# Performance work log

Hardware: AMD Instinct MI355X
Metric: run time of the kernel (lower is better)

The kernel has to match this reference:

```python
import jax, jax.numpy as jnp
import numpy as np

LN_EPS = 1e-5

def setup_inputs() -> dict:
    key = jax.random.key(0)
    k1, k2, k3, k4 = jax.random.split(key, 4)
    B, C_ct, C_b, N = 2, 128, 32, 180
    D = H = W = 24
    ct_feat = jax.random.normal(k1, (B, C_ct, D, H, W), dtype=jnp.float32)
    beam_stack = jax.random.normal(k2, (B, N, C_b, D, H, W), dtype=jnp.float32)
    # 1x1x1 Conv3d query projection == per-voxel linear map C_ct -> C_b
    q_w = jax.random.normal(k3, (C_b, C_ct), dtype=jnp.float32) * (1.0 / np.sqrt(C_ct))
    q_b = jnp.zeros((C_b,), dtype=jnp.float32)
    ln_gamma = jnp.ones((C_b,), dtype=jnp.float32)
    ln_beta = jnp.zeros((C_b,), dtype=jnp.float32)
    return {"ct_feat": ct_feat, "beam_stack": beam_stack, "q_w": q_w,
            "q_b": q_b, "ln_gamma": ln_gamma, "ln_beta": ln_beta}

def reference(ct_feat, beam_stack, q_w, q_b, ln_gamma, ln_beta):
    B, C_ct, D, H, W = ct_feat.shape
    _, N, C_b = beam_stack.shape[:3]
    V = D * H * W
    scale = C_b ** -0.5
    # query: 1x1x1 conv -> [B, V, C_b]
    q = jnp.einsum('oc,bcv->bvo', q_w, ct_feat.reshape(B, C_ct, V)) + q_b
    kv = beam_stack.reshape(B, N, C_b, V)  # [B, N, C_b, V]
    # per-voxel logits over N control points
    logits = jnp.einsum('bvc,bncv->bvn', q, kv) * scale  # [B, V, N]
    attn_w = jax.nn.softmax(logits, axis=-1)
    fused = jnp.einsum('bvn,bncv->bvc', attn_w, kv)  # [B, V, C_b]
    # LayerNorm over channel dim (eps matches torch default)
    mu = jnp.mean(fused, axis=-1, keepdims=True)
    var = jnp.mean(jnp.square(fused - mu), axis=-1, keepdims=True)
    fused = (fused - mu) * jax.lax.rsqrt(var + LN_EPS) * ln_gamma + ln_beta
    fused = fused.transpose(0, 2, 1).reshape(B, C_b, D, H, W)
    return fused, attn_w
```

## Files before the change

kernel.cpp:

```cpp
#include <hip/hip_runtime.h>
#include <math.h>

#define BB      2
#define C_CT    128
#define CB      32
#define NN      180
#define VV      13824
#define VOXB    64
#define GR      4
#define NPG     45
#define THREADS 256

typedef float vfloat4 __attribute__((ext_vector_type(4)));

__global__ __launch_bounds__(THREADS, 2)
void vmat_attn_kernel(const float* __restrict__ ct, const float* __restrict__ beam,
                      const float* __restrict__ qw, const float* __restrict__ qb,
                      const float* __restrict__ gam, const float* __restrict__ bet,
                      float* __restrict__ out)
{
    __shared__ __align__(16) float Wbuf[NN * VOXB];
    __shared__ __align__(16) float Pbuf[GR][CB][VOXB];
    __shared__ __align__(16) float l_part[GR][VOXB];
    __shared__ float l_final[VOXB];
    __shared__ float qb_s[CB], gam_s[CB], bet_s[CB];

    const int t    = threadIdx.x;
    const int lane = t & 63;
    const int g    = t >> 6;
    const int vq   = lane & 15;
    const int cg   = lane >> 4;
    const int bid  = blockIdx.x;
    const int b    = bid / (VV / VOXB);
    const int v0   = (bid % (VV / VOXB)) * VOXB;

    for (int i = t; i < CB * C_CT; i += THREADS) Wbuf[i] = qw[i];
    if (t < CB) { qb_s[t] = qb[t]; gam_s[t] = gam[t]; bet_s[t] = bet[t]; }
    __syncthreads();

    {
        const int v = v0 + lane;
        const float* ctp = ct + ((size_t)b * C_CT + g * 32) * VV + v;
        float ctv[32];
        #pragma unroll
        for (int j = 0; j < 32; ++j) ctv[j] = ctp[(size_t)j * VV];
        float qp[CB];
        #pragma unroll
        for (int o = 0; o < CB; ++o) qp[o] = 0.f;
        for (int j = 0; j < 32; ++j) {
            #pragma unroll
            for (int o = 0; o < CB; ++o)
                qp[o] = fmaf(Wbuf[o * C_CT + g * 32 + j], ctv[j], qp[o]);
        }
        #pragma unroll
        for (int o = 0; o < CB; ++o) Pbuf[g][o][lane] = qp[o];
    }
    __syncthreads();

    float q[8][4];
    #pragma unroll
    for (int ci = 0; ci < 8; ++ci) {
        const int o = cg * 8 + ci;
        float4 a0 = *reinterpret_cast<const float4*>(&Pbuf[0][o][vq * 4]);
        float4 a1 = *reinterpret_cast<const float4*>(&Pbuf[1][o][vq * 4]);
        float4 a2 = *reinterpret_cast<const float4*>(&Pbuf[2][o][vq * 4]);
        float4 a3 = *reinterpret_cast<const float4*>(&Pbuf[3][o][vq * 4]);
        q[ci][0] = a0.x + a1.x + a2.x + a3.x + qb_s[o];
        q[ci][1] = a0.y + a1.y + a2.y + a3.y + qb_s[o];
        q[ci][2] = a0.z + a1.z + a2.z + a3.z + qb_s[o];
        q[ci][3] = a0.w + a1.w + a2.w + a3.w + qb_s[o];
    }
    __syncthreads();

    const float scale = 0.17677669529663687f;
    float acc[8][4];
    #pragma unroll
    for (int ci = 0; ci < 8; ++ci)
        acc[ci][0] = acc[ci][1] = acc[ci][2] = acc[ci][3] = 0.f;
    float l0 = 0.f, l1 = 0.f, l2 = 0.f, l3 = 0.f;
    const float* bp0 = beam + (((size_t)b * NN + g * NPG) * CB + cg * 8) * VV + v0 + vq * 4;

    vfloat4 kvA[8], kvB[8];
    auto loadK = [&](vfloat4* kv, int i) {
        const float* bp = bp0 + (size_t)i * CB * VV;
        #pragma unroll
        for (int ci = 0; ci < 8; ++ci)
            kv[ci] = __builtin_nontemporal_load(
                reinterpret_cast<const vfloat4*>(bp + (size_t)ci * VV));
    };
    auto computeK = [&](const vfloat4* kv, int i) {
        float p0 = 0.f, p1 = 0.f, p2 = 0.f, p3 = 0.f;
        #pragma unroll
        for (int ci = 0; ci < 8; ++ci) {
            p0 = fmaf(q[ci][0], kv[ci].x, p0);
            p1 = fmaf(q[ci][1], kv[ci].y, p1);
            p2 = fmaf(q[ci][2], kv[ci].z, p2);
            p3 = fmaf(q[ci][3], kv[ci].w, p3);
        }
        p0 += __shfl_xor(p0, 16); p1 += __shfl_xor(p1, 16);
        p2 += __shfl_xor(p2, 16); p3 += __shfl_xor(p3, 16);
        p0 += __shfl_xor(p0, 32); p1 += __shfl_xor(p1, 32);
        p2 += __shfl_xor(p2, 32); p3 += __shfl_xor(p3, 32);
        float w0 = __expf(fminf(p0 * scale, 60.f));
        float w1 = __expf(fminf(p1 * scale, 60.f));
        float w2 = __expf(fminf(p2 * scale, 60.f));
        float w3 = __expf(fminf(p3 * scale, 60.f));
        if (cg == 0) {
            float4 wv; wv.x = w0; wv.y = w1; wv.z = w2; wv.w = w3;
            *reinterpret_cast<float4*>(&Wbuf[(g * NPG + i) * VOXB + vq * 4]) = wv;
        }
        l0 += w0; l1 += w1; l2 += w2; l3 += w3;
        #pragma unroll
        for (int ci = 0; ci < 8; ++ci) {
            acc[ci][0] = fmaf(w0, kv[ci].x, acc[ci][0]);
            acc[ci][1] = fmaf(w1, kv[ci].y, acc[ci][1]);
            acc[ci][2] = fmaf(w2, kv[ci].z, acc[ci][2]);
            acc[ci][3] = fmaf(w3, kv[ci].w, acc[ci][3]);
        }
    };

    loadK(kvA, 0);
    #pragma unroll 1
    for (int i = 0; i < NPG - 1; i += 2) {
        loadK(kvB, i + 1);
        computeK(kvA, i);
        if (i + 2 < NPG) loadK(kvA, i + 2);
        computeK(kvB, i + 1);
    }
    computeK(kvA, NPG - 1);

    #pragma unroll
    for (int ci = 0; ci < 8; ++ci) {
        float4 av; av.x = acc[ci][0]; av.y = acc[ci][1]; av.z = acc[ci][2]; av.w = acc[ci][3];
        *reinterpret_cast<float4*>(&Pbuf[g][cg * 8 + ci][vq * 4]) = av;
    }
    if (cg == 0) {
        float4 lv; lv.x = l0; lv.y = l1; lv.z = l2; lv.w = l3;
        *reinterpret_cast<float4*>(&l_part[g][vq * 4]) = lv;
    }
    __syncthreads();

    if (t < VOXB) {
        float lt = l_part[0][t] + l_part[1][t] + l_part[2][t] + l_part[3][t];
        l_final[t] = lt;
        float inv_l = 1.f / lt;
        float f[CB], mu = 0.f;
        #pragma unroll
        for (int c = 0; c < CB; ++c) {
            f[c] = (Pbuf[0][c][t] + Pbuf[1][c][t] + Pbuf[2][c][t] + Pbuf[3][c][t]) * inv_l;
            mu += f[c];
        }
        mu *= (1.f / CB);
        float var = 0.f;
        #pragma unroll
        for (int c = 0; c < CB; ++c) { float d = f[c] - mu; var = fmaf(d, d, var); }
        float rs = rsqrtf(var * (1.f / CB) + 1e-5f);
        float* op = out + (size_t)b * CB * VV + v0 + t;
        #pragma unroll
        for (int c = 0; c < CB; ++c)
            op[(size_t)c * VV] = (f[c] - mu) * rs * gam_s[c] + bet_s[c];
    }
    __syncthreads();

    {
        const int vv = t & 63;
        const int j  = t >> 6;
        const float inv_l = 1.f / l_final[vv];
        float* arow = out + (size_t)BB * CB * VV + ((size_t)b * VV + v0 + vv) * NN;
        const int q4_begin = j * 12;
        const int q4_end   = (j == 3) ? 45 : (j * 12 + 12);
        for (int q4 = q4_begin; q4 < q4_end; ++q4) {
            const int n0 = q4 * 4;
            float4 val;
            val.x = Wbuf[(n0 + 0) * VOXB + vv] * inv_l;
            val.y = Wbuf[(n0 + 1) * VOXB + vv] * inv_l;
            val.z = Wbuf[(n0 + 2) * VOXB + vv] * inv_l;
            val.w = Wbuf[(n0 + 3) * VOXB + vv] * inv_l;
            *reinterpret_cast<float4*>(arow + n0) = val;
        }
    }
}

extern "C" void kernel_launch(void* const* d_in, const int* in_sizes, int n_in,
                              void* d_out, int out_size, void* d_ws, size_t ws_size,
                              hipStream_t stream) {
    (void)in_sizes; (void)n_in; (void)out_size; (void)d_ws; (void)ws_size;
    const float* ct   = (const float*)d_in[0];
    const float* beam = (const float*)d_in[1];
    const float* qw   = (const float*)d_in[2];
    const float* qb   = (const float*)d_in[3];
    const float* gam  = (const float*)d_in[4];
    const float* bet  = (const float*)d_in[5];
    float* out = (float*)d_out;
    dim3 grid(BB * (VV / VOXB));
    vmat_attn_kernel<<<grid, THREADS, 0, stream>>>(ct, beam, qw, qb, gam, bet, out);
}
```

Measured before the change: 142.6 us.

## Split fused attention into projection, streaming, and combine kernels via workspace

Splits the single fused kernel into three: a query-projection kernel, a 64-thread streaming kernel that handles one quarter of the control points per block, and a combine kernel that merges partial accumulators, applies LayerNorm and normalizes attention weights in place. The goal is to raise the number of blocks and wavefronts in flight so more beam-stack loads are outstanding, and the streaming loop moves to triple buffering. The cost is extra global traffic: queries are staged in the output buffer, and partials plus unnormalized weights take an extra round trip through memory. If the workspace is too small, the original fused kernel runs as a fallback.

After: 191.4 us. 34.3% more time.

```diff
diff --git a/kernel.cpp b/kernel.cpp
--- a/kernel.cpp
+++ b/kernel.cpp
@@ -6,38 +6,229 @@
 #define CB      32
 #define NN      180
 #define VV      13824
-#define VOXB    64
-#define GR      4
 #define NPG     45
-#define THREADS 256
+#define SCALE   0.17677669529663687f
 
 typedef float vfloat4 __attribute__((ext_vector_type(4)));
 
-__global__ __launch_bounds__(THREADS, 2)
-void vmat_attn_kernel(const float* __restrict__ ct, const float* __restrict__ beam,
-                      const float* __restrict__ qw, const float* __restrict__ qb,
-                      const float* __restrict__ gam, const float* __restrict__ bet,
-                      float* __restrict__ out)
+__global__ __launch_bounds__(256, 2)
+void qproj_kernel(const float* __restrict__ ct, const float* __restrict__ qw,
+                  const float* __restrict__ qb, float* __restrict__ qout)
 {
-    __shared__ __align__(16) float Wbuf[NN * VOXB];
-    __shared__ __align__(16) float Pbuf[GR][CB][VOXB];
-    __shared__ __align__(16) float l_part[GR][VOXB];
-    __shared__ float l_final[VOXB];
+    __shared__ float qw_t[C_CT * 33];
+    __shared__ __align__(16) float ct_s[C_CT * 64];
+    __shared__ float q_s[64 * 33];
+    __shared__ float qb_s[CB];
+    const int t  = threadIdx.x;
+    const int b  = blockIdx.x / 216;
+    const int v0 = (blockIdx.x % 216) * 64;
+
+    for (int i = t; i < CB * C_CT; i += 256) {
+        const int o = i >> 7, c = i & 127;
+        qw_t[c * 33 + o] = qw[i];
+    }
+    {
+        const float* ctbase = ct + (size_t)b * C_CT * VV + v0;
+        for (int i = t; i < C_CT * 16; i += 256) {
+            const int c = i >> 4, k = i & 15;
+            *reinterpret_cast<vfloat4*>(&ct_s[c * 64 + k * 4]) =
+                *reinterpret_cast<const vfloat4*>(ctbase + (size_t)c * VV + k * 4);
+        }
+    }
+    if (t < CB) qb_s[t] = qb[t];
+    __syncthreads();
+
+    const int o = t & 31, va = t >> 5;
+    float a[8];
+    #pragma unroll
+    for (int k = 0; k < 8; ++k) a[k] = qb_s[o];
+    for (int kc = 0; kc < C_CT; ++kc) {
+        const float wk = qw_t[kc * 33 + o];
+        const float* cr = &ct_s[kc * 64];
+        #pragma unroll
+        for (int k = 0; k < 8; ++k) a[k] = fmaf(wk, cr[va + 8 * k], a[k]);
+    }
+    #pragma unroll
+    for (int k = 0; k < 8; ++k) q_s[(va + 8 * k) * 33 + o] = a[k];
+    __syncthreads();
+
+    for (int i = t; i < CB * 64; i += 256) {
+        const int c = i >> 6, v = i & 63;
+        qout[((size_t)b * CB + c) * VV + v0 + v] = q_s[v * 33 + c];
+    }
+}
+
+__global__ __launch_bounds__(64, 2)
+void stream_kernel(const float* __restrict__ beam, const float* __restrict__ qarr,
+                   float* __restrict__ wout, float* __restrict__ ws_acc,
+                   float* __restrict__ ws_l)
+{
+    const int u  = blockIdx.x;
+    const int b  = u / 864;
+    const int r  = u % 864;
+    const int g  = r & 3;
+    const int v0 = (r >> 2) * 64;
+    const int lane = threadIdx.x;
+    const int vq = lane & 15;
+    const int cg = lane >> 4;
+
+    float q[8][4];
+    #pragma unroll
+    for (int ci = 0; ci < 8; ++ci) {
+        vfloat4 qv = *reinterpret_cast<const vfloat4*>(
+            qarr + ((size_t)b * CB + cg * 8 + ci) * VV + v0 + vq * 4);
+        q[ci][0] = qv.x; q[ci][1] = qv.y; q[ci][2] = qv.z; q[ci][3] = qv.w;
+    }
+
+    float acc[8][4];
+    #pragma unroll
+    for (int ci = 0; ci < 8; ++ci)
+        acc[ci][0] = acc[ci][1] = acc[ci][2] = acc[ci][3] = 0.f;
+    float l0 = 0.f, l1 = 0.f, l2 = 0.f, l3 = 0.f;
+
+    const float* bpc  = beam + (((size_t)b * NN + g * NPG) * CB + cg * 8) * VV + v0 + vq * 4;
+    float*       wrow = wout + ((size_t)b * VV + v0 + vq * 4) * NN + g * NPG;
+
+    vfloat4 kvA[8], kvB[8], kvC[8];
+    auto loadK = [&](vfloat4* kv, int i) {
+        const float* p = bpc + (size_t)i * (CB * VV);
+        #pragma unroll
+        for (int ci = 0; ci < 8; ++ci)
+            kv[ci] = __builtin_nontemporal_load(
+                reinterpret_cast<const vfloat4*>(p + (size_t)ci * VV));
+    };
+    auto computeK = [&](const vfloat4* kv, int i) {
+        float p0 = 0.f, p1 = 0.f, p2 = 0.f, p3 = 0.f;
+        #pragma unroll
+        for (int ci = 0; ci < 8; ++ci) {
+            p0 = fmaf(q[ci][0], kv[ci].x, p0);
+            p1 = fmaf(q[ci][1], kv[ci].y, p1);
+            p2 = fmaf(q[ci][2], kv[ci].z, p2);
+            p3 = fmaf(q[ci][3], kv[ci].w, p3);
+        }
+        p0 += __shfl_xor(p0, 16); p1 += __shfl_xor(p1, 16);
+        p2 += __shfl_xor(p2, 16); p3 += __shfl_xor(p3, 16);
+        p0 += __shfl_xor(p0, 32); p1 += __shfl_xor(p1, 32);
+        p2 += __shfl_xor(p2, 32); p3 += __shfl_xor(p3, 32);
+        const float w0 = __expf(fminf(p0 * SCALE, 60.f));
+        const float w1 = __expf(fminf(p1 * SCALE, 60.f));
+        const float w2 = __expf(fminf(p2 * SCALE, 60.f));
+        const float w3 = __expf(fminf(p3 * SCALE, 60.f));
+        if (cg == 0) {
+            wrow[0 * NN + i] = w0;
+            wrow[1 * NN + i] = w1;
+            wrow[2 * NN + i] = w2;
+            wrow[3 * NN + i] = w3;
+        }
+        l0 += w0; l1 += w1; l2 += w2; l3 += w3;
+        #pragma unroll
+        for (int ci = 0; ci < 8; ++ci) {
+            acc[ci][0] = fmaf(w0, kv[ci].x, acc[ci][0]);
+            acc[ci][1] = fmaf(w1, kv[ci].y, acc[ci][1]);
+            acc[ci][2] = fmaf(w2, kv[ci].z, acc[ci][2]);
+            acc[ci][3] = fmaf(w3, kv[ci].w, acc[ci][3]);
+        }
+    };
+
+    loadK(kvA, 0);
+    loadK(kvB, 1);
+    #pragma unroll 1
+    for (int i = 0; i < NPG; i += 3) {
+        loadK(kvC, i + 2);
+        computeK(kvA, i);
+        if (i + 3 < NPG) loadK(kvA, i + 3);
+        computeK(kvB, i + 1);
+        if (i + 4 < NPG) loadK(kvB, i + 4);
+        computeK(kvC, i + 2);
+    }
+
+    #pragma unroll
+    for (int ci = 0; ci < 8; ++ci) {
+        vfloat4 a; a.x = acc[ci][0]; a.y = acc[ci][1]; a.z = acc[ci][2]; a.w = acc[ci][3];
+        *reinterpret_cast<vfloat4*>(
+            ws_acc + (((size_t)b * 4 + g) * CB + cg * 8 + ci) * VV + v0 + vq * 4) = a;
+    }
+    if (cg == 0) {
+        vfloat4 lv; lv.x = l0; lv.y = l1; lv.z = l2; lv.w = l3;
+        *reinterpret_cast<vfloat4*>(ws_l + ((size_t)b * 4 + g) * VV + v0 + vq * 4) = lv;
+    }
+}
+
+__global__ __launch_bounds__(256, 4)
+void combine_kernel(const float* __restrict__ ws_acc, const float* __restrict__ ws_l,
+                    const float* __restrict__ gam, const float* __restrict__ bet,
+                    float* __restrict__ out)
+{
+    __shared__ float il_s[32];
+    const int t  = threadIdx.x;
+    const int b  = blockIdx.x / 432;
+    const int v0 = (blockIdx.x % 432) * 32;
+
+    if (t < 32) {
+        const int v = v0 + t;
+        float lt = 0.f;
+        #pragma unroll
+        for (int g = 0; g < 4; ++g) lt += ws_l[((size_t)b * 4 + g) * VV + v];
+        const float il = 1.f / lt;
+        il_s[t] = il;
+        float f[CB], mu = 0.f;
+        #pragma unroll
+        for (int c = 0; c < CB; ++c) {
+            float s = 0.f;
+            #pragma unroll
+            for (int g = 0; g < 4; ++g)
+                s += ws_acc[(((size_t)b * 4 + g) * CB + c) * VV + v];
+            f[c] = s * il;
+            mu += f[c];
+        }
+        mu *= (1.f / CB);
+        float var = 0.f;
+        #pragma unroll
+        for (int c = 0; c < CB; ++c) { const float d = f[c] - mu; var = fmaf(d, d, var); }
+        const float rs = rsqrtf(var * (1.f / CB) + 1e-5f);
+        float* op = out + (size_t)b * CB * VV + v;
+        #pragma unroll
+        for (int c = 0; c < CB; ++c)
+            op[(size_t)c * VV] = (f[c] - mu) * rs * gam[c] + bet[c];
+    }
+    __syncthreads();
+
+    {
+        const int v  = t >> 3;
+        const int kk = t & 7;
+        const float il = il_s[v];
+        float* arow = out + (size_t)BB * CB * VV + ((size_t)b * VV + v0 + v) * NN;
+        #pragma unroll
+        for (int m = 0; m < 6; ++m) {
+            const int q4 = kk + m * 8;
+            if (q4 < NN / 4) {
+                vfloat4 wv = *reinterpret_cast<const vfloat4*>(arow + q4 * 4);
+                wv.x *= il; wv.y *= il; wv.z *= il; wv.w *= il;
+                *reinterpret_cast<vfloat4*>(arow + q4 * 4) = wv;
+            }
+        }
+    }
+}
+
+__global__ __launch_bounds__(256, 2)
+void vmat_attn_fallback(const float* __restrict__ ct, const float* __restrict__ beam,
+                        const float* __restrict__ qw, const float* __restrict__ qb,
+                        const float* __restrict__ gam, const float* __restrict__ bet,
+                        float* __restrict__ out)
+{
+    __shared__ __align__(16) float Wbuf[NN * 64];
+    __shared__ __align__(16) float Pbuf[4][CB][64];
+    __shared__ __align__(16) float l_part[4][64];
+    __shared__ float l_final[64];
     __shared__ float qb_s[CB], gam_s[CB], bet_s[CB];
 
-    const int t    = threadIdx.x;
-    const int lane = t & 63;
-    const int g    = t >> 6;
-    const int vq   = lane & 15;
-    const int cg   = lane >> 4;
-    const int bid  = blockIdx.x;
-    const int b    = bid / (VV / VOXB);
-    const int v0   = (bid % (VV / VOXB)) * VOXB;
-
-    for (int i = t; i < CB * C_CT; i += THREADS) Wbuf[i] = qw[i];
+    const int t = threadIdx.x, lane = t & 63, g = t >> 6;
+    const int vq = lane & 15, cg = lane >> 4;
+    const int bid = blockIdx.x, b = bid / 216, v0 = (bid % 216) * 64;
+
+    for (int i = t; i < CB * C_CT; i += 256) Wbuf[i] = qw[i];
     if (t < CB) { qb_s[t] = qb[t]; gam_s[t] = gam[t]; bet_s[t] = bet[t]; }
     __syncthreads();
-
     {
         const int v = v0 + lane;
         const float* ctp = ct + ((size_t)b * C_CT + g * 32) * VV + v;
@@ -56,30 +247,26 @@
         for (int o = 0; o < CB; ++o) Pbuf[g][o][lane] = qp[o];
     }
     __syncthreads();
-
     float q[8][4];
     #pragma unroll
     for (int ci = 0; ci < 8; ++ci) {
         const int o = cg * 8 + ci;
-        float4 a0 = *reinterpret_cast<const float4*>(&Pbuf[0][o][vq * 4]);
-        float4 a1 = *reinterpret_cast<const float4*>(&Pbuf[1][o][vq * 4]);
-        float4 a2 = *reinterpret_cast<const float4*>(&Pbuf[2][o][vq * 4]);
-        float4 a3 = *reinterpret_cast<const float4*>(&Pbuf[3][o][vq * 4]);
+        vfloat4 a0 = *reinterpret_cast<const vfloat4*>(&Pbuf[0][o][vq * 4]);
+        vfloat4 a1 = *reinterpret_cast<const vfloat4*>(&Pbuf[1][o][vq * 4]);
+        vfloat4 a2 = *reinterpret_cast<const vfloat4*>(&Pbuf[2][o][vq * 4]);
+        vfloat4 a3 = *reinterpret_cast<const vfloat4*>(&Pbuf[3][o][vq * 4]);
         q[ci][0] = a0.x + a1.x + a2.x + a3.x + qb_s[o];
         q[ci][1] = a0.y + a1.y + a2.y + a3.y + qb_s[o];
         q[ci][2] = a0.z + a1.z + a2.z + a3.z + qb_s[o];
         q[ci][3] = a0.w + a1.w + a2.w + a3.w + qb_s[o];
     }
     __syncthreads();
-
-    const float scale = 0.17677669529663687f;
     float acc[8][4];
     #pragma unroll
     for (int ci = 0; ci < 8; ++ci)
         acc[ci][0] = acc[ci][1] = acc[ci][2] = acc[ci][3] = 0.f;
     float l0 = 0.f, l1 = 0.f, l2 = 0.f, l3 = 0.f;
     const float* bp0 = beam + (((size_t)b * NN + g * NPG) * CB + cg * 8) * VV + v0 + vq * 4;
-
     vfloat4 kvA[8], kvB[8];
     auto loadK = [&](vfloat4* kv, int i) {
         const float* bp = bp0 + (size_t)i * CB * VV;
@@ -101,13 +288,13 @@
         p2 += __shfl_xor(p2, 16); p3 += __shfl_xor(p3, 16);
         p0 += __shfl_xor(p0, 32); p1 += __shfl_xor(p1, 32);
         p2 += __shfl_xor(p2, 32); p3 += __shfl_xor(p3, 32);
-        float w0 = __expf(fminf(p0 * scale, 60.f));
-        float w1 = __expf(fminf(p1 * scale, 60.f));
-        float w2 = __expf(fminf(p2 * scale, 60.f));
-        float w3 = __expf(fminf(p3 * scale, 60.f));
+        float w0 = __expf(fminf(p0 * SCALE, 60.f));
+        float w1 = __expf(fminf(p1 * SCALE, 60.f));
+        float w2 = __expf(fminf(p2 * SCALE, 60.f));
+        float w3 = __expf(fminf(p3 * SCALE, 60.f));
         if (cg == 0) {
-            float4 wv; wv.x = w0; wv.y = w1; wv.z = w2; wv.w = w3;
-            *reinterpret_cast<float4*>(&Wbuf[(g * NPG + i) * VOXB + vq * 4]) = wv;
+            vfloat4 wv; wv.x = w0; wv.y = w1; wv.z = w2; wv.w = w3;
+            *reinterpret_cast<vfloat4*>(&Wbuf[(g * NPG + i) * 64 + vq * 4]) = wv;
         }
         l0 += w0; l1 += w1; l2 += w2; l3 += w3;
         #pragma unroll
@@ -118,7 +305,6 @@
             acc[ci][3] = fmaf(w3, kv[ci].w, acc[ci][3]);
         }
     };
-
     loadK(kvA, 0);
     #pragma unroll 1
     for (int i = 0; i < NPG - 1; i += 2) {
@@ -128,19 +314,17 @@
         computeK(kvB, i + 1);
     }
     computeK(kvA, NPG - 1);
-
     #pragma unroll
     for (int ci = 0; ci < 8; ++ci) {
-        float4 av; av.x = acc[ci][0]; av.y = acc[ci][1]; av.z = acc[ci][2]; av.w = acc[ci][3];
-        *reinterpret_cast<float4*>(&Pbuf[g][cg * 8 + ci][vq * 4]) = av;
+        vfloat4 a; a.x = acc[ci][0]; a.y = acc[ci][1]; a.z = acc[ci][2]; a.w = acc[ci][3];
+        *reinterpret_cast<vfloat4*>(&Pbuf[g][cg * 8 + ci][vq * 4]) = a;
     }
     if (cg == 0) {
-        float4 lv; lv.x = l0; lv.y = l1; lv.z = l2; lv.w = l3;
-        *reinterpret_cast<float4*>(&l_part[g][vq * 4]) = lv;
-    }
-    __syncthreads();
-
-    if (t < VOXB) {
+        vfloat4 lv; lv.x = l0; lv.y = l1; lv.z = l2; lv.w = l3;
+        *reinterpret_cast<vfloat4*>(&l_part[g][vq * 4]) = lv;
+    }
+    __syncthreads();
+    if (t < 64) {
         float lt = l_part[0][t] + l_part[1][t] + l_part[2][t] + l_part[3][t];
         l_final[t] = lt;
         float inv_l = 1.f / lt;
@@ -161,22 +345,19 @@
             op[(size_t)c * VV] = (f[c] - mu) * rs * gam_s[c] + bet_s[c];
     }
     __syncthreads();
-
     {
-        const int vv = t & 63;
-        const int j  = t >> 6;
+        const int vv = t & 63, j = t >> 6;
         const float inv_l = 1.f / l_final[vv];
         float* arow = out + (size_t)BB * CB * VV + ((size_t)b * VV + v0 + vv) * NN;
-        const int q4_begin = j * 12;
-        const int q4_end   = (j == 3) ? 45 : (j * 12 + 12);
-        for (int q4 = q4_begin; q4 < q4_end; ++q4) {
+        const int q4b = j * 12, q4e = (j == 3) ? 45 : (j * 12 + 12);
+        for (int q4 = q4b; q4 < q4e; ++q4) {
             const int n0 = q4 * 4;
-            float4 val;
-            val.x = Wbuf[(n0 + 0) * VOXB + vv] * inv_l;
-            val.y = Wbuf[(n0 + 1) * VOXB + vv] * inv_l;
-            val.z = Wbuf[(n0 + 2) * VOXB + vv] * inv_l;
-            val.w = Wbuf[(n0 + 3) * VOXB + vv] * inv_l;
-            *reinterpret_cast<float4*>(arow + n0) = val;
+            vfloat4 val;
+            val.x = Wbuf[(n0 + 0) * 64 + vv] * inv_l;
+            val.y = Wbuf[(n0 + 1) * 64 + vv] * inv_l;
+            val.z = Wbuf[(n0 + 2) * 64 + vv] * inv_l;
+            val.w = Wbuf[(n0 + 3) * 64 + vv] * inv_l;
+            *reinterpret_cast<vfloat4*>(arow + n0) = val;
         }
     }
 }
@@ -184,7 +365,7 @@
 extern "C" void kernel_launch(void* const* d_in, const int* in_sizes, int n_in,
                               void* d_out, int out_size, void* d_ws, size_t ws_size,
                               hipStream_t stream) {
-    (void)in_sizes; (void)n_in; (void)out_size; (void)d_ws; (void)ws_size;
+    (void)in_sizes; (void)n_in; (void)out_size;
     const float* ct   = (const float*)d_in[0];
     const float* beam = (const float*)d_in[1];
     const float* qw   = (const float*)d_in[2];
@@ -192,6 +373,20 @@
     const float* gam  = (const float*)d_in[4];
     const float* bet  = (const float*)d_in[5];
     float* out = (float*)d_out;
-    dim3 grid(BB * (VV / VOXB));
-    vmat_attn_kernel<<<grid, THREADS, 0, stream>>>(ct, beam, qw, qb, gam, bet, out);
-}
+
+    const size_t ACC_FLOATS = (size_t)BB * 4 * CB * VV;
+    const size_t L_FLOATS   = (size_t)BB * 4 * VV;
+    const size_t WS_NEEDED  = (ACC_FLOATS + L_FLOATS) * sizeof(float);
+
+    if (ws_size >= WS_NEEDED) {
+        float* ws_acc = (float*)d_ws;
+        float* ws_l   = ws_acc + ACC_FLOATS;
+        float* qarr   = out;
+        float* wout   = out + (size_t)BB * CB * VV;
+        qproj_kernel  <<<dim3(BB * 216),  256, 0, stream>>>(ct, qw, qb, qarr);
+        stream_kernel <<<dim3(BB * 864),   64, 0, stream>>>(beam, qarr, wout, ws_acc, ws_l);
+        combine_kernel<<<dim3(BB * 432),  256, 0, stream>>>(ws_acc, ws_l, gam, bet, out);
+    } else {
+        vmat_attn_fallback<<<dim3(BB * 216), 256, 0, stream>>>(ct, beam, qw, qb, gam, bet, out);
+    }
+}
```
